# Kernel optimization log

Hardware: AMD Instinct MI355X
Metric: run time of the kernel (lower is better)

Reference implementation:

```python
import jax, jax.numpy as jnp
import numpy as np

LEN_SORT_WINDOW = 2


def _butterfly_indices(v_len, d_v):
    # Column j is arange rolled right by s_j: s_0 = s_1 = 0, s_j = 2*(j-1) mod v_len.
    # (The butterfly_factor_to_matrix result in the original code is discarded;
    #  only the cyclic shifts matter.)
    shifts = np.zeros(d_v, dtype=np.int64)
    if d_v > 1:
        shifts[1:] = (LEN_SORT_WINDOW * np.arange(d_v - 1, dtype=np.int64)) % v_len
    rows = np.arange(v_len, dtype=np.int64)[:, None]
    return jnp.asarray((rows - shifts[None, :]) % v_len)  # [v_len, d_v] int64


def setup_inputs() -> dict:
    key = jax.random.key(0)
    B, L, D = 8, 4096, 1024
    v = jax.random.normal(key, (B, L, D), dtype=jnp.float32)
    return {"v": v}


def reference(v) -> jnp.ndarray:
    B, L, D = v.shape
    idx = _butterfly_indices(L, D)                       # [L, D]
    # gather: v_shifted[b,i,j] = v[b, idx[i,j], j]
    v_shifted = jnp.take_along_axis(v, jnp.broadcast_to(idx[None], (B, L, D)), axis=1)
    # windowed pairwise sort (ascending, window = 2) along the sequence dim
    pairs = v_shifted.reshape(B, L // LEN_SORT_WINDOW, LEN_SORT_WINDOW, D)
    v_sorted = jnp.sort(pairs, axis=2)
    return v_sorted.reshape(B, L, D)
```

## Files before the change

### kernel.cpp

```cpp
#include <hip/hip_runtime.h>

namespace {

constexpr int B  = 8;
constexpr int L  = 4096;
constexpr int D  = 1024;
constexpr int D4 = D / 4;
constexpr int P  = L / 2;
constexpr int TJ = 32;
constexpr int TP = 64;
constexpr int RP = TP + TJ;
constexpr int RR = 2 * RP;
constexpr int NT = 512;
constexpr int NW = NT / 64;
constexpr int T  = 4;
constexpr int NCH = RR * TJ * 4 / 1024;
constexpr int CPW = NCH / NW;
static_assert(CPW == 3, "vmcnt literal below assumes 3 in-flight chunk loads");
static_assert(2 * RR * TJ * 4 <= 49152, "LDS must stay well under 64 KiB");

__device__ __forceinline__ void async_ld16(const float* g, float* l) {
  __builtin_amdgcn_global_load_lds(
      (const __attribute__((address_space(1))) void*)g,
      (__attribute__((address_space(3))) void*)l, 16, 0, 0);
}

__global__ __launch_bounds__(NT, 6)
void swd_kernel(const float* __restrict__ v, float4* __restrict__ out) {
  const int j0 = blockIdx.x * TJ;
  const int ty = blockIdx.y;
  const int b  = blockIdx.z;

  __shared__ float lds[2][RR * TJ];

  const int tid  = threadIdx.x;
  const int wave = tid >> 6;
  const int lane = tid & 63;

  const float* __restrict__ vb = v + (size_t)b * L * D + j0;

  const int f  = lane & 7;
  const int kb = wave * 8 + (lane >> 3);

  const int g   = tid & 7;
  const int c   = tid >> 3;
  const int krb = 2 * c - 8 * g + 2 * (TJ - 1) - 6;
  const bool sp = (j0 == 0) && (g == 0);

  float4* __restrict__ ob = out + (size_t)b * L * D4 + (j0 >> 2) + g;

  auto stage = [&](int tt, int s) {
    const int p0 = tt * TP;
    const int r0 = p0 - (j0 + TJ - 2);
#pragma unroll
    for (int i = 0; i < CPW; ++i) {
      const int kr  = kb + 64 * i;
      const int q   = (r0 + (kr >> 1)) & (P - 1);
      const int row = 2 * q + (kr & 1);
      async_ld16(vb + (size_t)row * D + 4 * f,
                 &lds[s][(wave + NW * i) * (8 * TJ)]);
    }
  };

  const int tt0 = ty * T;
  stage(tt0, 0);

#pragma unroll
  for (int t = 0; t < T; ++t) {
    if (t + 1 < T) {
      stage(tt0 + t + 1, (t + 1) & 1);
      asm volatile("s_waitcnt vmcnt(3)" ::: "memory");
    } else {
      asm volatile("s_waitcnt vmcnt(0)" ::: "memory");
    }
    __builtin_amdgcn_s_barrier();
    asm volatile("" ::: "memory");

    const float* Lb = lds[t & 1];

    float4 m[4], M[4];
#pragma unroll
    for (int u = 0; u < 4; ++u) {
      const float4 a0 = *(const float4*)&Lb[(krb + 2 * u)     * TJ + 4 * g];
      const float4 a1 = *(const float4*)&Lb[(krb + 2 * u + 1) * TJ + 4 * g];
      m[u].x = fminf(a0.x, a1.x); M[u].x = fmaxf(a0.x, a1.x);
      m[u].y = fminf(a0.y, a1.y); M[u].y = fmaxf(a0.y, a1.y);
      m[u].z = fminf(a0.z, a1.z); M[u].z = fmaxf(a0.z, a1.z);
      m[u].w = fminf(a0.w, a1.w); M[u].w = fmaxf(a0.w, a1.w);
    }

    float4 e, o;
    e.x = sp ? m[2].x : m[3].x; e.y = m[2].y; e.z = m[1].z; e.w = m[0].w;
    o.x = sp ? M[2].x : M[3].x; o.y = M[2].y; o.z = M[1].z; o.w = M[0].w;

    const size_t ro = (size_t)(2 * ((tt0 + t) * TP + c)) * D4;
    ob[ro]      = e;
    ob[ro + D4] = o;

    asm volatile("s_waitcnt lgkmcnt(0)" ::: "memory");
    __builtin_amdgcn_s_barrier();
    asm volatile("" ::: "memory");
  }
}

}

extern "C" void kernel_launch(void* const* d_in, const int* , int ,
                              void* d_out, int , void* , size_t ,
                              hipStream_t stream) {
  const float* v = (const float*)d_in[0];
  float4* out = (float4*)d_out;
  dim3 grid(D / TJ, P / (T * TP), B);
  swd_kernel<<<grid, NT, 0, stream>>>(v, out);
}
```

Before: 242.9 us.

## Use wider column tiles with single-shot load and drop double-buffered pipeline

Changes the tile shape to 64 columns by 32 pairs. Each block now loads its whole halo tile into LDS once with async global-to-LDS loads, then sorts and stores, instead of looping over four sequence tiles with double-buffered staging. Because the halo depends on the column width, the ratio of halo rows to useful rows grows (RP=96 for TP=32), so redundant reads from global memory increase. Block count rises and each block uses 48 KiB of LDS, which limits occupancy to about three blocks per CU, and there is no intra-block overlap of load and compute.

```diff
diff --git a/kernel.cpp b/kernel.cpp
--- a/kernel.cpp
+++ b/kernel.cpp
@@ -7,17 +7,16 @@
 constexpr int D  = 1024;
 constexpr int D4 = D / 4;
 constexpr int P  = L / 2;
-constexpr int TJ = 32;
-constexpr int TP = 64;
+constexpr int TJ = 64;
+constexpr int TP = 32;
 constexpr int RP = TP + TJ;
 constexpr int RR = 2 * RP;
 constexpr int NT = 512;
 constexpr int NW = NT / 64;
-constexpr int T  = 4;
 constexpr int NCH = RR * TJ * 4 / 1024;
 constexpr int CPW = NCH / NW;
-static_assert(CPW == 3, "vmcnt literal below assumes 3 in-flight chunk loads");
-static_assert(2 * RR * TJ * 4 <= 49152, "LDS must stay well under 64 KiB");
+static_assert(CPW == 6, "chunk math");
+static_assert(RR * TJ * 4 == 48 * 1024, "LDS = 48 KiB, 3 blocks/CU");
 
 __device__ __forceinline__ void async_ld16(const float* g, float* l) {
   __builtin_amdgcn_global_load_lds(
@@ -28,79 +27,55 @@
 __global__ __launch_bounds__(NT, 6)
 void swd_kernel(const float* __restrict__ v, float4* __restrict__ out) {
   const int j0 = blockIdx.x * TJ;
-  const int ty = blockIdx.y;
+  const int p0 = blockIdx.y * TP;
   const int b  = blockIdx.z;
 
-  __shared__ float lds[2][RR * TJ];
+  __shared__ float lds[RR * TJ];
 
   const int tid  = threadIdx.x;
   const int wave = tid >> 6;
   const int lane = tid & 63;
 
   const float* __restrict__ vb = v + (size_t)b * L * D + j0;
+  const int r0 = p0 - (j0 + TJ - 2);
 
-  const int f  = lane & 7;
-  const int kb = wave * 8 + (lane >> 3);
+  const int f  = lane & 15;
+  const int rc = lane >> 4;
+#pragma unroll
+  for (int i = 0; i < CPW; ++i) {
+    const int C   = wave + NW * i;
+    const int kr  = 4 * C + rc;
+    const int q   = (r0 + (kr >> 1)) & (P - 1);
+    const int row = 2 * q + (kr & 1);
+    async_ld16(vb + (size_t)row * D + 4 * f, &lds[C * 256]);
+  }
+  asm volatile("s_waitcnt vmcnt(0)" ::: "memory");
+  __syncthreads();
 
-  const int g   = tid & 7;
-  const int c   = tid >> 3;
+  const int g = tid & 15;
+  const int c = tid >> 4;
   const int krb = 2 * c - 8 * g + 2 * (TJ - 1) - 6;
   const bool sp = (j0 == 0) && (g == 0);
 
+  float4 m[4], M[4];
+#pragma unroll
+  for (int u = 0; u < 4; ++u) {
+    const float4 a0 = *(const float4*)&lds[(krb + 2 * u)     * TJ + 4 * g];
+    const float4 a1 = *(const float4*)&lds[(krb + 2 * u + 1) * TJ + 4 * g];
+    m[u].x = fminf(a0.x, a1.x); M[u].x = fmaxf(a0.x, a1.x);
+    m[u].y = fminf(a0.y, a1.y); M[u].y = fmaxf(a0.y, a1.y);
+    m[u].z = fminf(a0.z, a1.z); M[u].z = fmaxf(a0.z, a1.z);
+    m[u].w = fminf(a0.w, a1.w); M[u].w = fmaxf(a0.w, a1.w);
+  }
+
+  float4 e, o;
+  e.x = sp ? m[2].x : m[3].x; e.y = m[2].y; e.z = m[1].z; e.w = m[0].w;
+  o.x = sp ? M[2].x : M[3].x; o.y = M[2].y; o.z = M[1].z; o.w = M[0].w;
+
   float4* __restrict__ ob = out + (size_t)b * L * D4 + (j0 >> 2) + g;
-
-  auto stage = [&](int tt, int s) {
-    const int p0 = tt * TP;
-    const int r0 = p0 - (j0 + TJ - 2);
-#pragma unroll
-    for (int i = 0; i < CPW; ++i) {
-      const int kr  = kb + 64 * i;
-      const int q   = (r0 + (kr >> 1)) & (P - 1);
-      const int row = 2 * q + (kr & 1);
-      async_ld16(vb + (size_t)row * D + 4 * f,
-                 &lds[s][(wave + NW * i) * (8 * TJ)]);
-    }
-  };
-
-  const int tt0 = ty * T;
-  stage(tt0, 0);
-
-#pragma unroll
-  for (int t = 0; t < T; ++t) {
-    if (t + 1 < T) {
-      stage(tt0 + t + 1, (t + 1) & 1);
-      asm volatile("s_waitcnt vmcnt(3)" ::: "memory");
-    } else {
-      asm volatile("s_waitcnt vmcnt(0)" ::: "memory");
-    }
-    __builtin_amdgcn_s_barrier();
-    asm volatile("" ::: "memory");
-
-    const float* Lb = lds[t & 1];
-
-    float4 m[4], M[4];
-#pragma unroll
-    for (int u = 0; u < 4; ++u) {
-      const float4 a0 = *(const float4*)&Lb[(krb + 2 * u)     * TJ + 4 * g];
-      const float4 a1 = *(const float4*)&Lb[(krb + 2 * u + 1) * TJ + 4 * g];
-      m[u].x = fminf(a0.x, a1.x); M[u].x = fmaxf(a0.x, a1.x);
-      m[u].y = fminf(a0.y, a1.y); M[u].y = fmaxf(a0.y, a1.y);
-      m[u].z = fminf(a0.z, a1.z); M[u].z = fmaxf(a0.z, a1.z);
-      m[u].w = fminf(a0.w, a1.w); M[u].w = fmaxf(a0.w, a1.w);
-    }
-
-    float4 e, o;
-    e.x = sp ? m[2].x : m[3].x; e.y = m[2].y; e.z = m[1].z; e.w = m[0].w;
-    o.x = sp ? M[2].x : M[3].x; o.y = M[2].y; o.z = M[1].z; o.w = M[0].w;
-
-    const size_t ro = (size_t)(2 * ((tt0 + t) * TP + c)) * D4;
-    ob[ro]      = e;
-    ob[ro + D4] = o;
-
-    asm volatile("s_waitcnt lgkmcnt(0)" ::: "memory");
-    __builtin_amdgcn_s_barrier();
-    asm volatile("" ::: "memory");
-  }
+  const size_t ro = (size_t)(2 * (p0 + c)) * D4;
+  ob[ro]      = e;
+  ob[ro + D4] = o;
 }
 
 }
@@ -110,6 +85,6 @@
                               hipStream_t stream) {
   const float* v = (const float*)d_in[0];
   float4* out = (float4*)d_out;
-  dim3 grid(D / TJ, P / (T * TP), B);
+  dim3 grid(D / TJ, P / TP, B);
   swd_kernel<<<grid, NT, 0, stream>>>(v, out);
 }
```

Measured after the change: 233.5 us. 1.04x faster.
